# Kernel optimization log

Measured on AMD Instinct MI355X. Metric: run time of the kernel, lower is better.

The kernel has to match this reference:

```python
import jax, jax.numpy as jnp
import numpy as np

B, S, D, F, E = 4, 2048, 1024, 4096, 8
LN_EPS = 1e-5


def setup_inputs() -> dict:
    key = jax.random.key(0)
    ks = jax.random.split(key, 6)
    sc = 0.02
    return {
        "x": jax.random.normal(ks[0], (B, S, D), dtype=jnp.float32),
        "Wr": jax.random.normal(ks[1], (D, E), dtype=jnp.float32) * sc,
        "br": jnp.zeros((E,), jnp.float32),
        "ln_g": jnp.ones((D,), jnp.float32),
        "ln_b": jnp.zeros((D,), jnp.float32),
        "W1": jax.random.normal(ks[2], (E, D, F), dtype=jnp.float32) * sc,
        "b1": jnp.zeros((E, F), jnp.float32),
        "W2": jax.random.normal(ks[3], (E, F, D), dtype=jnp.float32) * sc,
        "b2": jnp.zeros((E, D), jnp.float32),
    }


def reference(x, Wr, br, ln_g, ln_b, W1, b1, W2, b2):
    tokens_shape = x.shape[:-1]
    xt = x.reshape(-1, x.shape[-1])  # [T, D]

    # top-1 routing (eval mode: no jitter noise, no dropout)
    router_logits = xt @ Wr + br                      # [T, E]
    router_probs = jax.nn.softmax(router_logits, axis=-1)
    gates = jnp.max(router_probs, axis=-1, keepdims=True)   # [T, 1]
    idx = jnp.argmax(router_probs, axis=-1)                 # [T] int
    onehot = jax.nn.one_hot(idx, E, dtype=xt.dtype)         # [T, E]

    # layernorm
    mu = jnp.mean(xt, axis=-1, keepdims=True)
    var = jnp.mean(jnp.square(xt - mu), axis=-1, keepdims=True)
    xn = (xt - mu) * jax.lax.rsqrt(var + LN_EPS) * ln_g + ln_b

    # expert FFN: per-token expert-specific GEMMs expressed via one-hot dispatch
    h = jnp.einsum('te,td,edf->tf', onehot, xn, W1) + b1[idx]  # [T, F]
    h = jax.nn.relu(h)
    y = jnp.einsum('te,tf,efd->td', onehot, h, W2) + b2[idx]   # [T, D]

    y = y * gates
    return y.reshape(tokens_shape + (y.shape[-1],))
```

## Files before the change

kernel.cpp:

```cpp
#include <hip/hip_runtime.h>
#include <stdint.h>

#define T_TOK 8192
#define DDIM  1024
#define FDIM  4096
#define NEXP  8
#define BM 128
#define BK 32
#define MAX_MT (T_TOK / BM + NEXP)

typedef __attribute__((ext_vector_type(8))) short bf16x8;
typedef __attribute__((ext_vector_type(8))) unsigned short u16x8;
typedef __attribute__((ext_vector_type(4))) float f32x4;

__device__ __forceinline__ unsigned short f2bf(float f) {
    union { float f; unsigned u; } v; v.f = f;
    unsigned u = v.u;
    u += 0x7fffu + ((u >> 16) & 1u);
    return (unsigned short)(u >> 16);
}

__device__ __forceinline__ void async16(const void* g, void* l) {
    __builtin_amdgcn_global_load_lds(
        (const __attribute__((address_space(1))) unsigned int*)g,
        (__attribute__((address_space(3))) unsigned int*)l, 16, 0, 0);
}

__global__ __launch_bounds__(256) void prep(
    const float* __restrict__ x, const float* __restrict__ Wr, const float* __restrict__ br,
    const float* __restrict__ lng, const float* __restrict__ lnb,
    const float* __restrict__ W1, const float* __restrict__ W2,
    unsigned short* __restrict__ xn, unsigned short* __restrict__ W1t,
    unsigned short* __restrict__ W2t, float* __restrict__ gate,
    int* __restrict__ expert, int* __restrict__ counts) {
    __shared__ float smem[64 * 65];
    int b = blockIdx.x, tid = threadIdx.x;

    if (b >= T_TOK) {
        int idx = b - T_TOK;
        const float* src; unsigned short* dst; int R, C, e, c0, r0;
        if (idx < 8192) {
            R = DDIM; C = FDIM;
            e = idx >> 10;
            c0 = (idx & 63) * 64; r0 = ((idx >> 6) & 15) * 64;
            src = W1; dst = W1t;
        } else {
            idx -= 8192;
            R = FDIM; C = DDIM;
            e = idx >> 10;
            c0 = (idx & 15) * 64; r0 = ((idx >> 4) & 63) * 64;
            src = W2; dst = W2t;
        }
        const float* s = src + (size_t)e * R * C;
        unsigned short* d = dst + (size_t)e * R * C;
        float (*tile)[65] = (float(*)[65])smem;
        int lr = tid >> 4, lc = (tid & 15) * 4;
#pragma unroll
        for (int i = 0; i < 4; i++) {
            float4 v = *(const float4*)&s[(size_t)(r0 + lr + i * 16) * C + c0 + lc];
            tile[lr + i * 16][lc + 0] = v.x;
            tile[lr + i * 16][lc + 1] = v.y;
            tile[lr + i * 16][lc + 2] = v.z;
            tile[lr + i * 16][lc + 3] = v.w;
        }
        __syncthreads();
#pragma unroll
        for (int i = 0; i < 2; i++) {
            int ix = tid + i * 256;
            int drow = ix >> 3, seg = ix & 7;
            u16x8 o;
#pragma unroll
            for (int j = 0; j < 8; j++) o[j] = f2bf(tile[seg * 8 + j][drow]);
            *(u16x8*)&d[(size_t)(c0 + drow) * R + r0 + seg * 8] = o;
        }
        return;
    }

    int t = b;
    const float4* xv4 = (const float4*)(x + (size_t)t * DDIM);
    float4 xv = xv4[tid];
    float s  = xv.x + xv.y + xv.z + xv.w;
    float sq = xv.x * xv.x + xv.y * xv.y + xv.z * xv.z + xv.w * xv.w;
    float lg[8] = {0, 0, 0, 0, 0, 0, 0, 0};
    const float4* wr4 = (const float4*)Wr;
    int d0 = tid * 4;
    const float* xr = (const float*)&xv;
#pragma unroll
    for (int r = 0; r < 4; r++) {
        float4 w0 = wr4[(d0 + r) * 2];
        float4 w1 = wr4[(d0 + r) * 2 + 1];
        lg[0] += xr[r] * w0.x; lg[1] += xr[r] * w0.y; lg[2] += xr[r] * w0.z; lg[3] += xr[r] * w0.w;
        lg[4] += xr[r] * w1.x; lg[5] += xr[r] * w1.y; lg[6] += xr[r] * w1.z; lg[7] += xr[r] * w1.w;
    }
#pragma unroll
    for (int o = 32; o > 0; o >>= 1) {
        s += __shfl_down(s, o); sq += __shfl_down(sq, o);
#pragma unroll
        for (int e = 0; e < 8; e++) lg[e] += __shfl_down(lg[e], o);
    }
    float* red = smem;
    float* bc = smem + 40;
    int lane = tid & 63, wv = tid >> 6;
    if (lane == 0) {
        red[wv * 10 + 0] = s; red[wv * 10 + 1] = sq;
#pragma unroll
        for (int e = 0; e < 8; e++) red[wv * 10 + 2 + e] = lg[e];
    }
    __syncthreads();
    if (tid == 0) {
        float S = 0, SQ = 0, L[8] = {0, 0, 0, 0, 0, 0, 0, 0};
        for (int w = 0; w < 4; w++) {
            S += red[w * 10 + 0]; SQ += red[w * 10 + 1];
            for (int e = 0; e < 8; e++) L[e] += red[w * 10 + 2 + e];
        }
        float mu = S * (1.f / DDIM);
        float var = SQ * (1.f / DDIM) - mu * mu;
        float rstd = rsqrtf(var + 1e-5f);
        int best = 0; float bl = -3.4e38f;
        for (int e = 0; e < 8; e++) {
            float l = L[e] + br[e];
            L[e] = l;
            if (l > bl) { bl = l; best = e; }
        }
        float den = 0;
        for (int e = 0; e < 8; e++) den += __expf(L[e] - bl);
        gate[t] = 1.f / den;
        expert[t] = best;
        atomicAdd(&counts[best], 1);
        bc[0] = mu; bc[1] = rstd;
    }
    __syncthreads();
    float mu = bc[0], rstd = bc[1];
    float4 gg = ((const float4*)lng)[tid];
    float4 bb = ((const float4*)lnb)[tid];
    ushort4 o;
    o.x = f2bf((xv.x - mu) * rstd * gg.x + bb.x);
    o.y = f2bf((xv.y - mu) * rstd * gg.y + bb.y);
    o.z = f2bf((xv.z - mu) * rstd * gg.z + bb.z);
    o.w = f2bf((xv.w - mu) * rstd * gg.w + bb.w);
    *(ushort4*)(xn + (size_t)t * DDIM + d0) = o;
}

__global__ __launch_bounds__(256) void scatter_perm(
    const int* __restrict__ expert, const int* __restrict__ counts,
    int* __restrict__ fill, int* __restrict__ perm) {
    __shared__ int offs_s[NEXP];
    if (threadIdx.x < NEXP) {
        int o = 0;
        for (int i = 0; i < (int)threadIdx.x; i++) o += counts[i];
        offs_s[threadIdx.x] = o;
    }
    __syncthreads();
    int t = blockIdx.x * 256 + threadIdx.x;
    int e = expert[t];
    int p = atomicAdd(&fill[e], 1);
    perm[offs_s[e] + p] = t;
}

template <int MODE>
__global__ __launch_bounds__(256) void gemm_grouped(
    const unsigned short* __restrict__ A, const unsigned short* __restrict__ Bt,
    const float* __restrict__ bias, unsigned short* __restrict__ Hout,
    float* __restrict__ Yout, const float* __restrict__ gate,
    const int* __restrict__ perm, const int* __restrict__ counts,
    int K, int N) {
    constexpr int BN_ = (MODE == 0) ? 128 : 64;
    constexpr int AI  = (MODE == 0) ? 4 : 2;
    constexpr int BROWS = (MODE == 0) ? 2 : 1;

    int rem = blockIdx.x;
    int e, off = 0, cnt = 0; bool found = false;
    for (e = 0; e < NEXP; e++) {
        cnt = counts[e];
        int mt = (cnt + (BM - 1)) >> 7;
        if (rem < mt) { found = true; break; }
        rem -= mt; off += cnt;
    }
    if (!found) return;
    int mbase = rem << 7;
    int mrem = cnt - mbase;
    int n0 = blockIdx.y * BN_;

    __shared__ __align__(16) unsigned short Alds[BM * BK];
    __shared__ __align__(16) unsigned short Blds[BN_ * BK];

    int tid = threadIdx.x;
    int lane = tid & 63, wave = tid >> 6;
    int grow = lane >> 2;
    int seg  = lane & 3;

    const unsigned short* ag[2];
    unsigned short* al[2];
    const unsigned short* bg[BROWS];
    unsigned short* bl[BROWS];
#pragma unroll
    for (int p = 0; p < 2; p++) {
        int r = p * 64 + wave * 16 + grow;
        int rr = (r < mrem) ? r : 0;
        if (MODE == 0) {
            int t = perm[off + mbase + rr];
            ag[p] = A + (size_t)t * K + seg * 8;
        } else {
            ag[p] = A + (size_t)(off + mbase + rr) * K + seg * 8;
        }
        al[p] = &Alds[(p * 64 + wave * 16) * BK];
    }
#pragma unroll
    for (int p = 0; p < BROWS; p++) {
        int r = p * 64 + wave * 16 + grow;
        bg[p] = Bt + ((size_t)e * N + n0 + r) * K + seg * 8;
        bl[p] = &Blds[(p * 64 + wave * 16) * BK];
    }

    int wr = (MODE == 0) ? (wave >> 1) * 64 : wave * 32;
    int wc = (MODE == 0) ? (wave & 1) * 64 : 0;
    int q = lane >> 4, l16 = lane & 15;

    f32x4 acc[AI][4] = {};

    for (int k0 = 0; k0 < K; k0 += BK) {
#pragma unroll
        for (int p = 0; p < 2; p++) async16(ag[p] + k0, al[p]);
#pragma unroll
        for (int p = 0; p < BROWS; p++) async16(bg[p] + k0, bl[p]);
        __syncthreads();
        bf16x8 af[AI], bfr[4];
#pragma unroll
        for (int i = 0; i < AI; i++)
            af[i] = *(const bf16x8*)&Alds[(wr + i * 16 + l16) * BK + q * 8];
#pragma unroll
        for (int j = 0; j < 4; j++)
            bfr[j] = *(const bf16x8*)&Blds[(wc + j * 16 + l16) * BK + q * 8];
#pragma unroll
        for (int i = 0; i < AI; i++)
#pragma unroll
            for (int j = 0; j < 4; j++)
                acc[i][j] = __builtin_amdgcn_mfma_f32_16x16x32_bf16(af[i], bfr[j], acc[i][j], 0, 0, 0);
        __syncthreads();
    }

    float bs[4];
#pragma unroll
    for (int j = 0; j < 4; j++) bs[j] = bias[(size_t)e * N + n0 + wc + j * 16 + l16];
#pragma unroll
    for (int i = 0; i < AI; i++) {
#pragma unroll
        for (int r = 0; r < 4; r++) {
            int lrow = wr + i * 16 + q * 4 + r;
            if (lrow < mrem) {
                if (MODE == 0) {
                    unsigned short* hp = Hout + (size_t)(off + mbase + lrow) * N + n0 + wc + l16;
#pragma unroll
                    for (int j = 0; j < 4; j++) {
                        float v = acc[i][j][r] + bs[j];
                        hp[j * 16] = f2bf(fmaxf(v, 0.f));
                    }
                } else {
                    int t = perm[off + mbase + lrow];
                    float gt = gate[t];
                    float* yp = Yout + (size_t)t * N + n0 + wc + l16;
#pragma unroll
                    for (int j = 0; j < 4; j++)
                        yp[j * 16] = (acc[i][j][r] + bs[j]) * gt;
                }
            }
        }
    }
}

extern "C" void kernel_launch(void* const* d_in, const int* in_sizes, int n_in,
                              void* d_out, int out_size, void* d_ws, size_t ws_size,
                              hipStream_t stream) {
    const float* x   = (const float*)d_in[0];
    const float* Wr  = (const float*)d_in[1];
    const float* br  = (const float*)d_in[2];
    const float* lng = (const float*)d_in[3];
    const float* lnb = (const float*)d_in[4];
    const float* W1  = (const float*)d_in[5];
    const float* b1  = (const float*)d_in[6];
    const float* W2  = (const float*)d_in[7];
    const float* b2  = (const float*)d_in[8];
    float* out = (float*)d_out;

    char* ws = (char*)d_ws;
    size_t o = 0;
    unsigned short* W1t = (unsigned short*)(ws + o); o += (size_t)NEXP * DDIM * FDIM * 2;
    unsigned short* W2t = (unsigned short*)(ws + o); o += (size_t)NEXP * DDIM * FDIM * 2;
    unsigned short* xn  = (unsigned short*)(ws + o); o += (size_t)T_TOK * DDIM * 2;
    unsigned short* h   = (unsigned short*)(ws + o); o += (size_t)T_TOK * FDIM * 2;
    float* gate = (float*)(ws + o); o += (size_t)T_TOK * 4;
    int* expert = (int*)(ws + o);   o += (size_t)T_TOK * 4;
    int* perm   = (int*)(ws + o);   o += (size_t)T_TOK * 4;
    int* meta   = (int*)(ws + o);
    int* counts = meta;
    int* fill   = meta + 8;

    hipMemsetAsync(meta, 0, 16 * sizeof(int), stream);

    prep<<<T_TOK + 16384, 256, 0, stream>>>(x, Wr, br, lng, lnb, W1, W2,
                                            xn, W1t, W2t, gate, expert, counts);
    scatter_perm<<<T_TOK / 256, 256, 0, stream>>>(expert, counts, fill, perm);
    gemm_grouped<0><<<dim3(MAX_MT, FDIM / 128), 256, 0, stream>>>(
        xn, W1t, b1, h, nullptr, nullptr, perm, counts, DDIM, FDIM);
    gemm_grouped<1><<<dim3(MAX_MT, DDIM / 64), 256, 0, stream>>>(
        h, W2t, b2, nullptr, out, gate, perm, counts, FDIM, DDIM);
}
```

Baseline: 714.4 us.

## Interleave token and weight-transpose blocks, transpose router weights for coalesced logits

Adds a small init kernel that zeroes the counters in place of the memset and transposes the router weights so each expert's column is contiguous. The prep kernel now interleaves token blocks with W1/W2 transpose blocks (b%3), so memory-bound transpose work and latency-bound token reductions share the GPU instead of running in separate phases. Router logits are computed by 32-lane groups per expert with coalesced loads. The layernorm statistics reduction is rewritten to go through shared memory. This adds an extra launch and some re-reading of x rows from global memory.

```diff
diff --git a/kernel.cpp b/kernel.cpp
--- a/kernel.cpp
+++ b/kernel.cpp
@@ -26,8 +26,16 @@
         (__attribute__((address_space(3))) unsigned int*)l, 16, 0, 0);
 }
 
+__global__ __launch_bounds__(256) void init_kernel(
+    const float* __restrict__ Wr, float* __restrict__ WrT, int* __restrict__ meta) {
+    int idx = blockIdx.x * 256 + threadIdx.x;
+    if (idx < 16) meta[idx] = 0;
+    float v = Wr[idx];
+    WrT[(idx & 7) * DDIM + (idx >> 3)] = v;
+}
+
 __global__ __launch_bounds__(256) void prep(
-    const float* __restrict__ x, const float* __restrict__ Wr, const float* __restrict__ br,
+    const float* __restrict__ x, const float* __restrict__ WrT, const float* __restrict__ br,
     const float* __restrict__ lng, const float* __restrict__ lnb,
     const float* __restrict__ W1, const float* __restrict__ W2,
     unsigned short* __restrict__ xn, unsigned short* __restrict__ W1t,
@@ -35,20 +43,19 @@
     int* __restrict__ expert, int* __restrict__ counts) {
     __shared__ float smem[64 * 65];
     int b = blockIdx.x, tid = threadIdx.x;
-
-    if (b >= T_TOK) {
-        int idx = b - T_TOK;
+    int r3 = b % 3, q = b / 3;
+
+    if (r3 != 0) {
         const float* src; unsigned short* dst; int R, C, e, c0, r0;
-        if (idx < 8192) {
+        if (r3 == 1) {
             R = DDIM; C = FDIM;
-            e = idx >> 10;
-            c0 = (idx & 63) * 64; r0 = ((idx >> 6) & 15) * 64;
+            e = q >> 10;
+            c0 = (q & 63) * 64; r0 = ((q >> 6) & 15) * 64;
             src = W1; dst = W1t;
         } else {
-            idx -= 8192;
             R = FDIM; C = DDIM;
-            e = idx >> 10;
-            c0 = (idx & 15) * 64; r0 = ((idx >> 4) & 63) * 64;
+            e = q >> 10;
+            c0 = (q & 15) * 64; r0 = ((q >> 4) & 63) * 64;
             src = W2; dst = W2t;
         }
         const float* s = src + (size_t)e * R * C;
@@ -76,61 +83,63 @@
         return;
     }
 
-    int t = b;
-    const float4* xv4 = (const float4*)(x + (size_t)t * DDIM);
-    float4 xv = xv4[tid];
+    int t = q;
+    const float* xrow = x + (size_t)t * DDIM;
+    float4 xv = ((const float4*)xrow)[tid];
     float s  = xv.x + xv.y + xv.z + xv.w;
     float sq = xv.x * xv.x + xv.y * xv.y + xv.z * xv.z + xv.w * xv.w;
-    float lg[8] = {0, 0, 0, 0, 0, 0, 0, 0};
-    const float4* wr4 = (const float4*)Wr;
-    int d0 = tid * 4;
-    const float* xr = (const float*)&xv;
-#pragma unroll
-    for (int r = 0; r < 4; r++) {
-        float4 w0 = wr4[(d0 + r) * 2];
-        float4 w1 = wr4[(d0 + r) * 2 + 1];
-        lg[0] += xr[r] * w0.x; lg[1] += xr[r] * w0.y; lg[2] += xr[r] * w0.z; lg[3] += xr[r] * w0.w;
-        lg[4] += xr[r] * w1.x; lg[5] += xr[r] * w1.y; lg[6] += xr[r] * w1.z; lg[7] += xr[r] * w1.w;
-    }
-#pragma unroll
-    for (int o = 32; o > 0; o >>= 1) {
-        s += __shfl_down(s, o); sq += __shfl_down(sq, o);
-#pragma unroll
-        for (int e = 0; e < 8; e++) lg[e] += __shfl_down(lg[e], o);
-    }
-    float* red = smem;
-    float* bc = smem + 40;
-    int lane = tid & 63, wv = tid >> 6;
-    if (lane == 0) {
-        red[wv * 10 + 0] = s; red[wv * 10 + 1] = sq;
-#pragma unroll
-        for (int e = 0; e < 8; e++) red[wv * 10 + 2 + e] = lg[e];
-    }
+    ((float2*)smem)[tid] = make_float2(s, sq);
+
+    int e = tid >> 5, l32 = tid & 31;
+    const float* wrow = WrT + e * DDIM + l32;
+    const float* xp = xrow + l32;
+    float a0 = 0, a1 = 0, a2 = 0, a3 = 0;
+#pragma unroll
+    for (int j = 0; j < 32; j += 4) {
+        a0 += xp[32 * j]       * wrow[32 * j];
+        a1 += xp[32 * (j + 1)] * wrow[32 * (j + 1)];
+        a2 += xp[32 * (j + 2)] * wrow[32 * (j + 2)];
+        a3 += xp[32 * (j + 3)] * wrow[32 * (j + 3)];
+    }
+    float acc = (a0 + a1) + (a2 + a3);
+#pragma unroll
+    for (int o = 16; o > 0; o >>= 1) acc += __shfl_down(acc, o, 32);
+    if ((tid & 31) == 0) smem[512 + e] = acc;
     __syncthreads();
-    if (tid == 0) {
-        float S = 0, SQ = 0, L[8] = {0, 0, 0, 0, 0, 0, 0, 0};
-        for (int w = 0; w < 4; w++) {
-            S += red[w * 10 + 0]; SQ += red[w * 10 + 1];
-            for (int e = 0; e < 8; e++) L[e] += red[w * 10 + 2 + e];
-        }
-        float mu = S * (1.f / DDIM);
-        float var = SQ * (1.f / DDIM) - mu * mu;
-        float rstd = rsqrtf(var + 1e-5f);
-        int best = 0; float bl = -3.4e38f;
-        for (int e = 0; e < 8; e++) {
-            float l = L[e] + br[e];
-            L[e] = l;
-            if (l > bl) { bl = l; best = e; }
-        }
-        float den = 0;
-        for (int e = 0; e < 8; e++) den += __expf(L[e] - bl);
-        gate[t] = 1.f / den;
-        expert[t] = best;
-        atomicAdd(&counts[best], 1);
-        bc[0] = mu; bc[1] = rstd;
+
+    if (tid < 64) {
+        float2 p0 = ((float2*)smem)[tid];
+        float2 p1 = ((float2*)smem)[tid + 64];
+        float2 p2 = ((float2*)smem)[tid + 128];
+        float2 p3 = ((float2*)smem)[tid + 192];
+        float ss = (p0.x + p1.x) + (p2.x + p3.x);
+        float qq = (p0.y + p1.y) + (p2.y + p3.y);
+#pragma unroll
+        for (int o = 32; o > 0; o >>= 1) {
+            ss += __shfl_down(ss, o);
+            qq += __shfl_down(qq, o);
+        }
+        if (tid == 0) {
+            float mu = ss * (1.f / DDIM);
+            float var = qq * (1.f / DDIM) - mu * mu;
+            float rstd = rsqrtf(var + 1e-5f);
+            int best = 0; float bl = -3.4e38f;
+            float L[8];
+            for (int k = 0; k < 8; k++) {
+                float l = smem[512 + k] + br[k];
+                L[k] = l;
+                if (l > bl) { bl = l; best = k; }
+            }
+            float den = 0;
+            for (int k = 0; k < 8; k++) den += __expf(L[k] - bl);
+            gate[t] = 1.f / den;
+            expert[t] = best;
+            atomicAdd(&counts[best], 1);
+            smem[520] = mu; smem[521] = rstd;
+        }
     }
     __syncthreads();
-    float mu = bc[0], rstd = bc[1];
+    float mu = smem[520], rstd = smem[521];
     float4 gg = ((const float4*)lng)[tid];
     float4 bb = ((const float4*)lnb)[tid];
     ushort4 o;
@@ -138,7 +147,7 @@
     o.y = f2bf((xv.y - mu) * rstd * gg.y + bb.y);
     o.z = f2bf((xv.z - mu) * rstd * gg.z + bb.z);
     o.w = f2bf((xv.w - mu) * rstd * gg.w + bb.w);
-    *(ushort4*)(xn + (size_t)t * DDIM + d0) = o;
+    *(ushort4*)(xn + (size_t)t * DDIM + tid * 4) = o;
 }
 
 __global__ __launch_bounds__(256) void scatter_perm(
@@ -289,16 +298,16 @@
     unsigned short* xn  = (unsigned short*)(ws + o); o += (size_t)T_TOK * DDIM * 2;
     unsigned short* h   = (unsigned short*)(ws + o); o += (size_t)T_TOK * FDIM * 2;
     float* gate = (float*)(ws + o); o += (size_t)T_TOK * 4;
+    float* WrT  = (float*)(ws + o); o += (size_t)NEXP * DDIM * 4;
     int* expert = (int*)(ws + o);   o += (size_t)T_TOK * 4;
     int* perm   = (int*)(ws + o);   o += (size_t)T_TOK * 4;
     int* meta   = (int*)(ws + o);
     int* counts = meta;
     int* fill   = meta + 8;
 
-    hipMemsetAsync(meta, 0, 16 * sizeof(int), stream);
-
-    prep<<<T_TOK + 16384, 256, 0, stream>>>(x, Wr, br, lng, lnb, W1, W2,
-                                            xn, W1t, W2t, gate, expert, counts);
+    init_kernel<<<32, 256, 0, stream>>>(Wr, WrT, meta);
+    prep<<<3 * T_TOK, 256, 0, stream>>>(x, WrT, br, lng, lnb, W1, W2,
+                                        xn, W1t, W2t, gate, expert, counts);
     scatter_perm<<<T_TOK / 256, 256, 0, stream>>>(expert, counts, fill, perm);
     gemm_grouped<0><<<dim3(MAX_MT, FDIM / 128), 256, 0, stream>>>(
         xn, W1t, b1, h, nullptr, nullptr, perm, counts, DDIM, FDIM);
```

Result: faster. 658.4 us (-7.8%).
